# Kernel tuning notes

Measured on AMD Instinct MI355X. Metric: run time of the kernel, lower is better.

The kernel has to match this reference:

```python
import jax, jax.numpy as jnp
import numpy as np

B, T, S, H, V, L = 64, 60, 60, 512, 32000, 2
NEG = -1.0e9  # matches torch mask value -1000000000.0


def setup_inputs() -> dict:
    key = jax.random.key(0)
    ks = jax.random.split(key, 12)
    sc = 0.05
    return {
        "indices": jax.random.randint(ks[0], (B, T), 0, V),
        "enc_output": jax.random.normal(ks[1], (B, S, H), dtype=jnp.float32),
        "de_lens": jax.random.randint(ks[2], (B,), 1, S + 1),
        "emb": jax.random.normal(ks[3], (V, H), dtype=jnp.float32) * sc,
        "w_ih": jax.random.normal(ks[4], (L, 4 * H, H), dtype=jnp.float32) * sc,
        "w_hh": jax.random.normal(ks[5], (L, 4 * H, H), dtype=jnp.float32) * sc,
        "b_ih": jnp.zeros((L, 4 * H), dtype=jnp.float32),
        "b_hh": jnp.zeros((L, 4 * H), dtype=jnp.float32),
        "lin_w": jax.random.normal(ks[6], (L, H, 2 * H), dtype=jnp.float32) * sc,
        "lin_b": jnp.zeros((L, H), dtype=jnp.float32),
        "out_w": jax.random.normal(ks[7], (V, H), dtype=jnp.float32) * sc,
        "out_b": jnp.zeros((V,), dtype=jnp.float32),
    }


def _lstm_seq(x, w_ih, w_hh, b_ih, b_hh):
    # x: [B,T,H] -> hidden states [B,T,H]; torch gate order i,f,g,o
    xg = jnp.einsum('bth,gh->btg', x, w_ih) + b_ih  # [B,T,4H]
    h0 = jnp.zeros((x.shape[0], w_hh.shape[1]), x.dtype)

    def step(carry, xg_t):
        h, c = carry
        g = xg_t + h @ w_hh.T + b_hh
        i, f, gg, o = jnp.split(g, 4, axis=-1)
        c = jax.nn.sigmoid(f) * c + jax.nn.sigmoid(i) * jnp.tanh(gg)
        h = jax.nn.sigmoid(o) * jnp.tanh(c)
        return (h, c), h

    _, hs = jax.lax.scan(step, (h0, h0), jnp.swapaxes(xg, 0, 1))
    return jnp.swapaxes(hs, 0, 1)


def reference(indices, enc_output, de_lens, emb, w_ih, w_hh, b_ih, b_hh,
              lin_w, lin_b, out_w, out_b):
    # additive length mask over encoder positions: [B,S]
    mask = jnp.where(jnp.arange(S)[None, :] < de_lens[:, None], 0.0, NEG).astype(enc_output.dtype)
    x = emb[indices]  # [B,T,H]
    for l in range(L):
        dec = _lstm_seq(x, w_ih[l], w_hh[l], b_ih[l], b_hh[l])  # [B,T,H]
        scores = jnp.einsum('bth,bsh->bts', dec, enc_output) + mask[:, None, :]
        probs = jax.nn.softmax(scores, axis=-1)
        attn = jnp.einsum('bts,bsh->bth', probs, enc_output)
        cat = jnp.concatenate([dec, attn], axis=-1)  # [B,T,2H]
        x = jnp.einsum('btk,hk->bth', cat, lin_w[l]) + lin_b[l]
    return jnp.einsum('bth,vh->btv', x, out_w) + out_b  # [B,T,V]
```

## Files before the change

### kernel.cpp

```cpp
#include <hip/hip_runtime.h>
#include <hip/hip_bf16.h>
#include <math.h>

#define B_ 64
#define T_ 60
#define S_ 60
#define H_ 512
#define V_ 32000
#define L_ 2
#define BT_ (B_*T_)
#define LDSROW 40
#define LDSROW2 72

typedef __attribute__((ext_vector_type(8))) short short8;
typedef __attribute__((ext_vector_type(4))) float f32x4;
typedef __attribute__((ext_vector_type(4))) unsigned int u32x4;

__device__ __forceinline__ short f2bf(float x) {
  __hip_bfloat16 h = __float2bfloat16(x);
  return __builtin_bit_cast(short, h);
}
__device__ __forceinline__ float bf2f(short s) {
  unsigned int u = ((unsigned int)(unsigned short)s) << 16;
  return __builtin_bit_cast(float, u);
}
__device__ __forceinline__ float sigm(float x) { return 1.f / (1.f + __expf(-x)); }
__device__ __forceinline__ float tanh_(float x) {
  float e = __expf(-2.f * fabsf(x));
  float t = (1.f - e) / (1.f + e);
  return x >= 0.f ? t : -t;
}

__device__ __forceinline__ void ld4g(const char* p, u32x4* q, bool llc) {
  if (llc)
    asm volatile("global_load_dwordx4 %0, %4, off sc0 sc1\n\t"
                 "global_load_dwordx4 %1, %4, off offset:16 sc0 sc1\n\t"
                 "global_load_dwordx4 %2, %4, off offset:32 sc0 sc1\n\t"
                 "global_load_dwordx4 %3, %4, off offset:48 sc0 sc1"
                 : "=v"(q[0]), "=v"(q[1]), "=v"(q[2]), "=v"(q[3]) : "v"(p));
  else
    asm volatile("global_load_dwordx4 %0, %4, off sc0\n\t"
                 "global_load_dwordx4 %1, %4, off offset:16 sc0\n\t"
                 "global_load_dwordx4 %2, %4, off offset:32 sc0\n\t"
                 "global_load_dwordx4 %3, %4, off offset:48 sc0"
                 : "=v"(q[0]), "=v"(q[1]), "=v"(q[2]), "=v"(q[3]) : "v"(p));
}

#define LDSBAR() do { \
    asm volatile("s_waitcnt lgkmcnt(0)" ::: "memory"); \
    __builtin_amdgcn_s_barrier(); \
    __builtin_amdgcn_sched_barrier(0); \
  } while (0)

__global__ __launch_bounds__(256) void convbf_k(const float* __restrict__ src,
                                                short* __restrict__ dst) {
  int g = blockIdx.x * 256 + threadIdx.x;
  const float* s = src + (size_t)g * 8;
  float4 v0 = *(const float4*)s, v1 = *(const float4*)(s + 4);
  short8 o;
  o[0]=f2bf(v0.x); o[1]=f2bf(v0.y); o[2]=f2bf(v0.z); o[3]=f2bf(v0.w);
  o[4]=f2bf(v1.x); o[5]=f2bf(v1.y); o[6]=f2bf(v1.z); o[7]=f2bf(v1.w);
  *(short8*)(dst + (size_t)g * 8) = o;
}

__global__ __launch_bounds__(256) void pack_whh_k(const float* __restrict__ whh,
                                                  short* __restrict__ pk) {
  int idx = blockIdx.x * 256 + threadIdx.x;
  int l = idx >> 17, rem = idx & 131071;
  int n = rem >> 6, k8 = rem & 63;
  int g = n >> 9, j = n & 511;
  int np = (j >> 4) * 64 + g * 16 + (j & 15);
  const float* src = whh + ((size_t)l * 2048 + n) * 512 + k8 * 8;
  float4 v0 = *(const float4*)src, v1 = *(const float4*)(src + 4);
  short8 o;
  o[0]=f2bf(v0.x); o[1]=f2bf(v0.y); o[2]=f2bf(v0.z); o[3]=f2bf(v0.w);
  o[4]=f2bf(v1.x); o[5]=f2bf(v1.y); o[6]=f2bf(v1.z); o[7]=f2bf(v1.w);
  size_t dst = (size_t)l * (2048 * 512) + ((size_t)((np >> 4) * 64 + k8)) * 128 + (np & 15) * 8;
  *(short8*)(pk + dst) = o;
}

__global__ __launch_bounds__(256) void embed_k(const int* __restrict__ idx,
                                               const float* __restrict__ emb,
                                               float* __restrict__ x) {
  int e = blockIdx.x * 256 + threadIdx.x;
  int bt = e >> 9, h = e & (H_ - 1);
  int row = idx[bt];
  x[e] = emb[(size_t)row * H_ + h];
}

template<bool XPOSE>
__global__ __launch_bounds__(256) void gemm_a32_k(
    const float* __restrict__ A, const float* __restrict__ Bw,
    const float* __restrict__ bias1, const float* __restrict__ bias2,
    float* __restrict__ C, short* __restrict__ Cbf, int M, int N, int K) {
  __shared__ short Ahs[128 * LDSROW];
  __shared__ short Als[128 * LDSROW];
  __shared__ short Bs[128 * LDSROW];
  int tid = threadIdx.x;
  int bm = blockIdx.y * 128, bn = blockIdx.x * 128;
  int wid = tid >> 6, lane = tid & 63;
  int wr = wid >> 1, wc = wid & 1;
  int lrow = lane & 15, lk = (lane >> 4) * 8;
  f32x4 acc[4][4];
#pragma unroll
  for (int i = 0; i < 4; ++i)
#pragma unroll
    for (int j = 0; j < 4; ++j) acc[i][j] = (f32x4){0.f, 0.f, 0.f, 0.f};

  int srow = tid >> 2, scol = (tid & 3) * 8;

  for (int k0 = 0; k0 < K; k0 += 32) {
#pragma unroll
    for (int it = 0; it < 2; ++it) {
      int r = srow + it * 64;
      const float* ap = A + (size_t)(bm + r) * K + k0 + scol;
      float4 a0 = *(const float4*)ap, a1 = *(const float4*)(ap + 4);
      float av[8] = {a0.x,a0.y,a0.z,a0.w,a1.x,a1.y,a1.z,a1.w};
      short8 hv, lv;
#pragma unroll
      for (int e = 0; e < 8; ++e) {
        short h = f2bf(av[e]);
        hv[e] = h;
        lv[e] = f2bf(av[e] - bf2f(h));
      }
      *(short8*)(Ahs + r * LDSROW + scol) = hv;
      *(short8*)(Als + r * LDSROW + scol) = lv;
      const float* bp = Bw + (size_t)(bn + r) * K + k0 + scol;
      float4 b0 = *(const float4*)bp, b1 = *(const float4*)(bp + 4);
      short8 bv;
      bv[0]=f2bf(b0.x); bv[1]=f2bf(b0.y); bv[2]=f2bf(b0.z); bv[3]=f2bf(b0.w);
      bv[4]=f2bf(b1.x); bv[5]=f2bf(b1.y); bv[6]=f2bf(b1.z); bv[7]=f2bf(b1.w);
      *(short8*)(Bs + r * LDSROW + scol) = bv;
    }
    __syncthreads();
    short8 ah[4], al[4], bfr[4];
#pragma unroll
    for (int i = 0; i < 4; ++i) {
      ah[i] = *(const short8*)(Ahs + (wr * 64 + i * 16 + lrow) * LDSROW + lk);
      al[i] = *(const short8*)(Als + (wr * 64 + i * 16 + lrow) * LDSROW + lk);
    }
#pragma unroll
    for (int j = 0; j < 4; ++j)
      bfr[j] = *(const short8*)(Bs + (wc * 64 + j * 16 + lrow) * LDSROW + lk);
#pragma unroll
    for (int i = 0; i < 4; ++i)
#pragma unroll
      for (int j = 0; j < 4; ++j) {
        acc[i][j] = __builtin_amdgcn_mfma_f32_16x16x32_bf16(ah[i], bfr[j], acc[i][j], 0, 0, 0);
        acc[i][j] = __builtin_amdgcn_mfma_f32_16x16x32_bf16(al[i], bfr[j], acc[i][j], 0, 0, 0);
      }
    __syncthreads();
  }

#pragma unroll
  for (int j = 0; j < 4; ++j) {
    int col = bn + wc * 64 + j * 16 + lrow;
    float bv = bias1[col] + (bias2 ? bias2[col] : 0.f);
#pragma unroll
    for (int i = 0; i < 4; ++i) {
#pragma unroll
      for (int r = 0; r < 4; ++r) {
        int row = bm + wr * 64 + i * 16 + (lane >> 4) * 4 + r;
        float v = acc[i][j][r] + bv;
        if (XPOSE) {
          int b = row / T_, t = row - b * T_;
          int g = col >> 9, jg = col & 511;
          int c8 = b >> 3, bloc = b & 7, q = jg >> 6;
          int nploc = ((jg >> 4) & 3) * 64 + g * 16 + (jg & 15);
          C[(((size_t)t * 64 + q * 8 + c8) * 8 + bloc) * 256 + nploc] = v;
        } else {
          C[(size_t)row * N + col] = v;
          if (Cbf) Cbf[(size_t)row * N + col] = f2bf(v);
        }
      }
    }
  }
}

__global__ __launch_bounds__(256) void gemm_bb_k(
    const short* __restrict__ A, const short* __restrict__ Bbf,
    const float* __restrict__ bias, float* __restrict__ C) {
  const int N = V_, K = H_;
  int n = blockIdx.x;
  int xcd = n & 7, pos = n >> 3;
  int base = (xcd < 4) ? xcd * 938 : 4 * 938 + (xcd - 4) * 937;
  int wg = base + pos;
  int bm = (wg % 30) * 128;
  int bn = (wg / 30) * 128;

  __shared__ short As[128 * LDSROW2];
  __shared__ short Bs[128 * LDSROW2];
  int tid = threadIdx.x;
  int wid = tid >> 6, lane = tid & 63;
  int wr = wid >> 1, wc = wid & 1;
  int lrow = lane & 15;
  f32x4 acc[4][4];
#pragma unroll
  for (int i = 0; i < 4; ++i)
#pragma unroll
    for (int j = 0; j < 4; ++j) acc[i][j] = (f32x4){0.f, 0.f, 0.f, 0.f};

  int srow = tid >> 2, scol = (tid & 3) * 16;

  for (int k0 = 0; k0 < K; k0 += 64) {
#pragma unroll
    for (int it = 0; it < 2; ++it) {
      int r = srow + it * 64;
      const short* ap = A + (size_t)(bm + r) * K + k0 + scol;
      short8 a0 = *(const short8*)ap, a1 = *(const short8*)(ap + 8);
      *(short8*)(As + r * LDSROW2 + scol) = a0;
      *(short8*)(As + r * LDSROW2 + scol + 8) = a1;
      const short* bp = Bbf + (size_t)(bn + r) * K + k0 + scol;
      short8 b0 = *(const short8*)bp, b1 = *(const short8*)(bp + 8);
      *(short8*)(Bs + r * LDSROW2 + scol) = b0;
      *(short8*)(Bs + r * LDSROW2 + scol + 8) = b1;
    }
    __syncthreads();
#pragma unroll
    for (int kk = 0; kk < 2; ++kk) {
      int lk = kk * 32 + (lane >> 4) * 8;
      short8 af[4], bfr[4];
#pragma unroll
      for (int i = 0; i < 4; ++i)
        af[i] = *(const short8*)(As + (wr * 64 + i * 16 + lrow) * LDSROW2 + lk);
#pragma unroll
      for (int j = 0; j < 4; ++j)
        bfr[j] = *(const short8*)(Bs + (wc * 64 + j * 16 + lrow) * LDSROW2 + lk);
#pragma unroll
      for (int i = 0; i < 4; ++i)
#pragma unroll
        for (int j = 0; j < 4; ++j)
          acc[i][j] = __builtin_amdgcn_mfma_f32_16x16x32_bf16(af[i], bfr[j], acc[i][j], 0, 0, 0);
    }
    __syncthreads();
  }

#pragma unroll
  for (int j = 0; j < 4; ++j) {
    int col = bn + wc * 64 + j * 16 + lrow;
    float bv = bias[col];
#pragma unroll
    for (int i = 0; i < 4; ++i)
#pragma unroll
      for (int r = 0; r < 4; ++r) {
        int row = bm + wr * 64 + i * 16 + (lane >> 4) * 4 + r;
        float v = acc[i][j][r] + bv;
        float* cp = C + (size_t)row * N + col;
        asm volatile("global_store_dword %0, %1, off nt" :: "v"(cp), "v"(v) : "memory");
      }
  }
}

__global__ __launch_bounds__(512, 2) void lstm_seq_k(
    const float* __restrict__ xg,
    const short* __restrict__ whh_pk,
    char* __restrict__ hx,
    float* __restrict__ dec) {
  __shared__ short hhi[16][520];
  __shared__ short hlo[16][520];
  __shared__ float gates[256][20];
  const int tid = threadIdx.x;
  const int bid = blockIdx.x;
  const int c = bid & 7, q = bid >> 3;
  const int w = tid >> 6, lane = tid & 63;
  const int lr = lane & 15, lkg = lane >> 4;

  for (int i = tid; i < 16 * 520; i += 512) {
    ((short*)hhi)[i] = 0;
    ((short*)hlo)[i] = 0;
  }

  short8 wreg[2][16];
#pragma unroll
  for (int nt = 0; nt < 2; ++nt)
#pragma unroll
    for (int kt = 0; kt < 16; ++kt)
      wreg[nt][kt] = *(const short8*)(whh_pk +
          ((size_t)((q * 16 + w * 2 + nt) * 64 + kt * 4 + lkg)) * 128 + lr * 8);

  const int bloc_e = tid & 7;
  const int p_e = (tid >> 3) & 31;
  const int j0 = p_e * 2;
  float cc0 = 0.f, cc1 = 0.f;

  char* grp = hx + (size_t)c * 65536;
  __syncthreads();

  for (int t = 0; t < T_; ++t) {
    const unsigned tgt = (unsigned)t;
    const char* pth = grp + (size_t)(t & 1) * 32768 + tid * 64;
    u32x4 qg[4];
    ld4g(pth, qg, false);
    for (unsigned a = 0;; ++a) {
      asm volatile("s_waitcnt vmcnt(0)" ::: "memory");
      __builtin_amdgcn_sched_barrier(0);
      unsigned bad = (qg[0][2] ^ tgt) | (qg[1][2] ^ tgt) |
                     (qg[2][2] ^ tgt) | (qg[3][2] ^ tgt);
      if (!bad) break;
      __builtin_amdgcn_s_sleep(1);
      ld4g(pth, qg, (a & 1) != 0);
    }
    u32x4 hiv = {qg[0][0], qg[1][0], qg[2][0], qg[3][0]};
    u32x4 lov = {qg[0][1], qg[1][1], qg[2][1], qg[3][1]};
    *(u32x4*)(&hhi[tid >> 6][(tid & 63) * 8]) = hiv;
    *(u32x4*)(&hlo[tid >> 6][(tid & 63) * 8]) = lov;
    LDSBAR();

    f32x4 acc[2];
    acc[0] = (f32x4){0.f, 0.f, 0.f, 0.f};
    acc[1] = (f32x4){0.f, 0.f, 0.f, 0.f};
#pragma unroll
    for (int kt = 0; kt < 16; ++kt) {
      short8 ah = *(const short8*)(&hhi[lr][kt * 32 + lkg * 8]);
      short8 al = *(const short8*)(&hlo[lr][kt * 32 + lkg * 8]);
#pragma unroll
      for (int nt = 0; nt < 2; ++nt) {
        acc[nt] = __builtin_amdgcn_mfma_f32_16x16x32_bf16(ah, wreg[nt][kt], acc[nt], 0, 0, 0);
        acc[nt] = __builtin_amdgcn_mfma_f32_16x16x32_bf16(al, wreg[nt][kt], acc[nt], 0, 0, 0);
      }
    }
#pragma unroll
    for (int nt = 0; nt < 2; ++nt)
      *(f32x4*)(&gates[(w * 2 + nt) * 16 + lr][lkg * 4]) = acc[nt];
    LDSBAR();

    if (tid < 256) {
      const float* xb = xg + ((size_t)t * 64 + bid) * 2048 + bloc_e * 256;
      float2 xv[4];
      int rw0 = (j0 >> 4) * 64 + (j0 & 15);
#pragma unroll
      for (int g = 0; g < 4; ++g)
        xv[g] = *(const float2*)(xb + rw0 + g * 16);
      float gv0[4], gv1[4];
#pragma unroll
      for (int g = 0; g < 4; ++g) {
        int rw = rw0 + g * 16;
        gv0[g] = gates[rw][bloc_e] + xv[g].x;
        gv1[g] = gates[rw + 1][bloc_e] + xv[g].y;
      }
      float cn0 = sigm(gv0[1]) * cc0 + sigm(gv0[0]) * tanh_(gv0[2]);
      float hn0 = sigm(gv0[3]) * tanh_(cn0);
      cc0 = cn0;
      float cn1 = sigm(gv1[1]) * cc1 + sigm(gv1[0]) * tanh_(gv1[2]);
      float hn1 = sigm(gv1[3]) * tanh_(cn1);
      cc1 = cn1;
      short hi0 = f2bf(hn0), hi1 = f2bf(hn1);
      short lo0 = f2bf(hn0 - bf2f(hi0)), lo1 = f2bf(hn1 - bf2f(hi1));
      u32x4 hv;
      hv[0] = (unsigned)(unsigned short)hi0 | ((unsigned)(unsigned short)hi1 << 16);
      hv[1] = (unsigned)(unsigned short)lo0 | ((unsigned)(unsigned short)lo1 << 16);
      hv[2] = tgt + 1u;
      hv[3] = tgt + 1u;
      char* pb = grp + (size_t)((t + 1) & 1) * 32768 +
                 ((size_t)(bloc_e * 256 + q * 32 + p_e)) * 16;
      asm volatile("global_store_dwordx4 %0, %1, off sc0" :: "v"(pb), "v"(hv) : "memory");
      asm volatile("global_store_dwordx4 %0, %1, off sc0 sc1" :: "v"(pb), "v"(hv) : "memory");
      float2 dv; dv.x = hn0; dv.y = hn1;
      *(float2*)(dec + ((size_t)(c * 8 + bloc_e) * T_ + t) * H_ + q * 64 + j0) = dv;
    }
    LDSBAR();
  }
}

__global__ __launch_bounds__(256) void attn_k(const float* __restrict__ dec,
                                              const float* __restrict__ enc,
                                              const int* __restrict__ lens,
                                              float* __restrict__ cat) {
  int bt = blockIdx.x;
  int b = bt / T_;
  __shared__ float dsh[H_];
  __shared__ float p[64];
  int tid = threadIdx.x;
  dsh[tid] = dec[(size_t)bt * H_ + tid];
  dsh[tid + 256] = dec[(size_t)bt * H_ + tid + 256];
  __syncthreads();
  int wid = tid >> 6, lane = tid & 63;
  int len = lens[b];
  for (int s = wid; s < S_; s += 4) {
    const float* er = enc + ((size_t)(b * S_ + s)) * H_ + lane * 8;
    float4 e0 = *(const float4*)er, e1 = *(const float4*)(er + 4);
    const float* dr = dsh + lane * 8;
    float sum = e0.x*dr[0] + e0.y*dr[1] + e0.z*dr[2] + e0.w*dr[3]
              + e1.x*dr[4] + e1.y*dr[5] + e1.z*dr[6] + e1.w*dr[7];
#pragma unroll
    for (int off = 32; off > 0; off >>= 1) sum += __shfl_down(sum, off);
    if (lane == 0) p[s] = sum + (s < len ? 0.f : -1.0e9f);
  }
  __syncthreads();
  if (wid == 0) {
    float v = (lane < S_) ? p[lane] : -INFINITY;
    float m = v;
#pragma unroll
    for (int off = 32; off > 0; off >>= 1) m = fmaxf(m, __shfl_down(m, off));
    m = __shfl(m, 0);
    float e = (lane < S_) ? expf(v - m) : 0.f;
    float ssum = e;
#pragma unroll
    for (int off = 32; off > 0; off >>= 1) ssum += __shfl_down(ssum, off);
    ssum = __shfl(ssum, 0);
    if (lane < S_) p[lane] = e / ssum;
  }
  __syncthreads();
  int h = tid * 2;
  float a0 = 0.f, a1 = 0.f;
  for (int s = 0; s < S_; ++s) {
    float ps = p[s];
    const float* er = enc + ((size_t)(b * S_ + s)) * H_ + h;
    a0 += ps * er[0];
    a1 += ps * er[1];
  }
  size_t base = (size_t)bt * (2 * H_);
  cat[base + h]          = dsh[h];
  cat[base + h + 1]      = dsh[h + 1];
  cat[base + H_ + h]     = a0;
  cat[base + H_ + h + 1] = a1;
}

extern "C" void kernel_launch(void* const* d_in, const int* in_sizes, int n_in,
                              void* d_out, int out_size, void* d_ws, size_t ws_size,
                              hipStream_t stream) {
  (void)in_sizes; (void)n_in; (void)out_size; (void)ws_size;
  const int*   indices = (const int*)d_in[0];
  const float* enc     = (const float*)d_in[1];
  const int*   de_lens = (const int*)d_in[2];
  const float* emb     = (const float*)d_in[3];
  const float* w_ih    = (const float*)d_in[4];
  const float* w_hh    = (const float*)d_in[5];
  const float* b_ih    = (const float*)d_in[6];
  const float* b_hh    = (const float*)d_in[7];
  const float* lin_w   = (const float*)d_in[8];
  const float* lin_b   = (const float*)d_in[9];
  const float* out_w   = (const float*)d_in[10];
  const float* out_b   = (const float*)d_in[11];
  float* outp = (float*)d_out;

  char* ws = (char*)d_ws;
  size_t off = 0;
  auto alloc = [&](size_t bytes) -> void* {
    void* p = ws + off; off += (bytes + 255) & ~(size_t)255; return p;
  };
  float* x      = (float*)alloc((size_t)BT_ * H_ * 4);
  float* xg     = (float*)alloc((size_t)BT_ * 4 * H_ * 4);
  float* dec    = (float*)alloc((size_t)BT_ * H_ * 4);
  float* cat    = (float*)alloc((size_t)BT_ * 2 * H_ * 4);
  short* ow_bf  = (short*)alloc((size_t)V_ * H_ * 2);
  short* whh_pk = (short*)alloc((size_t)L_ * 4 * H_ * H_ * 2);
  short* x_bf   = (short*)alloc((size_t)BT_ * H_ * 2);
  char*  hx     = (char*)alloc((size_t)8 * 2 * 32768);

  convbf_k<<<V_ * H_ / 8 / 256, 256, 0, stream>>>(out_w, ow_bf);
  pack_whh_k<<<L_ * 2048 * 64 / 256, 256, 0, stream>>>(w_hh, whh_pk);
  embed_k<<<BT_ * H_ / 256, 256, 0, stream>>>(indices, emb, x);

  for (int l = 0; l < L_; ++l) {
    gemm_a32_k<true><<<dim3(4 * H_ / 128, BT_ / 128), 256, 0, stream>>>(
        x, w_ih + (size_t)l * 4 * H_ * H_, b_ih + l * 4 * H_, b_hh + l * 4 * H_,
        xg, nullptr, BT_, 4 * H_, H_);
    hipMemsetAsync(hx, 0, (size_t)8 * 2 * 32768, stream);
    lstm_seq_k<<<64, 512, 0, stream>>>(
        xg, whh_pk + (size_t)l * 4 * H_ * H_, hx, dec);
    attn_k<<<BT_, 256, 0, stream>>>(dec, enc, de_lens, cat);
    gemm_a32_k<false><<<dim3(H_ / 128, BT_ / 128), 256, 0, stream>>>(
        cat, lin_w + (size_t)l * H_ * 2 * H_, lin_b + l * H_, nullptr,
        x, (l == L_ - 1) ? x_bf : nullptr, BT_, H_, 2 * H_);
  }

  gemm_bb_k<<<30 * (V_ / 128), 256, 0, stream>>>(x_bf, ow_bf, out_b, outp);
}
```

Before: 974.3 us.

## Split LSTM waves into h-pollers and h-publishers, prefetch xg before polling

The recurrent LSTM kernel now gives its two halves of the workgroup separate jobs each step. Threads 0-255 prefetch their xg gate inputs and then poll and load twice as many hidden-state granules as before. Threads 256-511 publish the previous step's bf16 hi/lo hidden state, staged in a new LDS buffer, to the global exchange area. The aim is to take the xg load latency and the global publish stores off the critical path of the cross-block step handshake. In exchange, publishing moves one step later and the pollers carry more loads each, so the handoff latency between blocks may not shrink.

Result: slower. 1.157 ms (+18.8%).

```diff
diff --git a/kernel.cpp b/kernel.cpp
--- a/kernel.cpp
+++ b/kernel.cpp
@@ -259,6 +259,7 @@
   __shared__ short hhi[16][520];
   __shared__ short hlo[16][520];
   __shared__ float gates[256][20];
+  __shared__ unsigned hstg[2][256];
   const int tid = threadIdx.x;
   const int bid = blockIdx.x;
   const int c = bid & 7, q = bid >> 3;
@@ -278,32 +279,64 @@
       wreg[nt][kt] = *(const short8*)(whh_pk +
           ((size_t)((q * 16 + w * 2 + nt) * 64 + kt * 4 + lkg)) * 128 + lr * 8);
 
+  const bool ldw = (tid < 256);
   const int bloc_e = tid & 7;
   const int p_e = (tid >> 3) & 31;
   const int j0 = p_e * 2;
+  const int lbloc = tid >> 5;
+  const int lj16 = (tid & 31) * 16;
+  const int s = tid - 256;
+  const int sbloc = s & 7, sp = (s >> 3) & 31;
+  char* grp = hx + (size_t)c * 65536;
+  char* sgran = grp + ((size_t)(sbloc * 256 + q * 32 + sp)) * 16;
+
   float cc0 = 0.f, cc1 = 0.f;
-
-  char* grp = hx + (size_t)c * 65536;
   __syncthreads();
 
   for (int t = 0; t < T_; ++t) {
     const unsigned tgt = (unsigned)t;
-    const char* pth = grp + (size_t)(t & 1) * 32768 + tid * 64;
-    u32x4 qg[4];
-    ld4g(pth, qg, false);
-    for (unsigned a = 0;; ++a) {
-      asm volatile("s_waitcnt vmcnt(0)" ::: "memory");
-      __builtin_amdgcn_sched_barrier(0);
-      unsigned bad = (qg[0][2] ^ tgt) | (qg[1][2] ^ tgt) |
-                     (qg[2][2] ^ tgt) | (qg[3][2] ^ tgt);
-      if (!bad) break;
-      __builtin_amdgcn_s_sleep(1);
-      ld4g(pth, qg, (a & 1) != 0);
-    }
-    u32x4 hiv = {qg[0][0], qg[1][0], qg[2][0], qg[3][0]};
-    u32x4 lov = {qg[0][1], qg[1][1], qg[2][1], qg[3][1]};
-    *(u32x4*)(&hhi[tid >> 6][(tid & 63) * 8]) = hiv;
-    *(u32x4*)(&hlo[tid >> 6][(tid & 63) * 8]) = lov;
+    float2 xgv[4];
+    if (ldw) {
+      const float* xb = xg + ((size_t)t * 64 + bid) * 2048 + bloc_e * 256;
+      int rw0 = (j0 >> 4) * 64 + (j0 & 15);
+#pragma unroll
+      for (int g = 0; g < 4; ++g) xgv[g] = *(const float2*)(xb + rw0 + g * 16);
+      asm volatile("" ::: "memory");
+
+      const char* pth = grp + (size_t)(t & 1) * 32768 + (size_t)tid * 128;
+      u32x4 qg[8];
+      ld4g(pth, qg, false);
+      ld4g(pth + 64, qg + 4, false);
+      for (unsigned a = 0;; ++a) {
+        asm volatile("s_waitcnt vmcnt(0)" ::: "memory");
+        __builtin_amdgcn_sched_barrier(0);
+        unsigned bad = 0;
+#pragma unroll
+        for (int i = 0; i < 8; ++i) bad |= (qg[i][2] ^ tgt);
+        if (!bad) break;
+        __builtin_amdgcn_s_sleep(1);
+        bool llc = (a & 1) != 0;
+        ld4g(pth, qg, llc);
+        ld4g(pth + 64, qg + 4, llc);
+      }
+      u32x4 hi0 = {qg[0][0], qg[1][0], qg[2][0], qg[3][0]};
+      u32x4 hi1 = {qg[4][0], qg[5][0], qg[6][0], qg[7][0]};
+      u32x4 lo0 = {qg[0][1], qg[1][1], qg[2][1], qg[3][1]};
+      u32x4 lo1 = {qg[4][1], qg[5][1], qg[6][1], qg[7][1]};
+      *(u32x4*)(&hhi[lbloc][lj16])     = hi0;
+      *(u32x4*)(&hhi[lbloc][lj16 + 8]) = hi1;
+      *(u32x4*)(&hlo[lbloc][lj16])     = lo0;
+      *(u32x4*)(&hlo[lbloc][lj16 + 8]) = lo1;
+    } else if (t > 0) {
+      u32x4 hv;
+      hv[0] = hstg[0][s];
+      hv[1] = hstg[1][s];
+      hv[2] = tgt;
+      hv[3] = tgt;
+      char* pb = sgran + (size_t)(t & 1) * 32768;
+      asm volatile("global_store_dwordx4 %0, %1, off sc0" :: "v"(pb), "v"(hv) : "memory");
+      asm volatile("global_store_dwordx4 %0, %1, off sc0 sc1" :: "v"(pb), "v"(hv) : "memory");
+    }
     LDSBAR();
 
     f32x4 acc[2];
@@ -324,19 +357,14 @@
       *(f32x4*)(&gates[(w * 2 + nt) * 16 + lr][lkg * 4]) = acc[nt];
     LDSBAR();
 
-    if (tid < 256) {
-      const float* xb = xg + ((size_t)t * 64 + bid) * 2048 + bloc_e * 256;
-      float2 xv[4];
+    if (ldw) {
+      float gv0[4], gv1[4];
       int rw0 = (j0 >> 4) * 64 + (j0 & 15);
-#pragma unroll
-      for (int g = 0; g < 4; ++g)
-        xv[g] = *(const float2*)(xb + rw0 + g * 16);
-      float gv0[4], gv1[4];
 #pragma unroll
       for (int g = 0; g < 4; ++g) {
         int rw = rw0 + g * 16;
-        gv0[g] = gates[rw][bloc_e] + xv[g].x;
-        gv1[g] = gates[rw + 1][bloc_e] + xv[g].y;
+        gv0[g] = gates[rw][bloc_e] + xgv[g].x;
+        gv1[g] = gates[rw + 1][bloc_e] + xgv[g].y;
       }
       float cn0 = sigm(gv0[1]) * cc0 + sigm(gv0[0]) * tanh_(gv0[2]);
       float hn0 = sigm(gv0[3]) * tanh_(cn0);
@@ -346,15 +374,10 @@
       cc1 = cn1;
       short hi0 = f2bf(hn0), hi1 = f2bf(hn1);
       short lo0 = f2bf(hn0 - bf2f(hi0)), lo1 = f2bf(hn1 - bf2f(hi1));
-      u32x4 hv;
-      hv[0] = (unsigned)(unsigned short)hi0 | ((unsigned)(unsigned short)hi1 << 16);
-      hv[1] = (unsigned)(unsigned short)lo0 | ((unsigned)(unsigned short)lo1 << 16);
-      hv[2] = tgt + 1u;
-      hv[3] = tgt + 1u;
-      char* pb = grp + (size_t)((t + 1) & 1) * 32768 +
-                 ((size_t)(bloc_e * 256 + q * 32 + p_e)) * 16;
-      asm volatile("global_store_dwordx4 %0, %1, off sc0" :: "v"(pb), "v"(hv) : "memory");
-      asm volatile("global_store_dwordx4 %0, %1, off sc0 sc1" :: "v"(pb), "v"(hv) : "memory");
+      hstg[0][tid] = (unsigned)(unsigned short)hi0 |
+                     ((unsigned)(unsigned short)hi1 << 16);
+      hstg[1][tid] = (unsigned)(unsigned short)lo0 |
+                     ((unsigned)(unsigned short)lo1 << 16);
       float2 dv; dv.x = hn0; dv.y = hn1;
       *(float2*)(dec + ((size_t)(c * 8 + bloc_e) * T_ + t) * H_ + q * 64 + j0) = dv;
     }
```
